# Optimization experiments

Hardware: AMD Instinct MI355X
Metric: run time of the kernel (lower is better)

The kernel has to match this reference:

```python
import jax, jax.numpy as jnp
import numpy as np

KS = (10, 25, 50, 100)  # numbers of highest-scored tiles to average (eval mode averages over all)
CLAMP = 1e4


def setup_inputs() -> dict:
    key = jax.random.key(0)
    k1, k2, k3, k4, k5, k6, k7 = jax.random.split(key, 7)
    B, C, N, H, O = 8, 2048, 8000, 256, 1000
    x = jax.random.normal(k1, (B, C, N), dtype=jnp.float32)
    # Conv1d(kernel=1) weights == [out, in] matrices
    W0 = jax.random.normal(k2, (H, C), dtype=jnp.float32) * (1.0 / np.sqrt(C))
    b0 = jax.random.normal(k3, (H,), dtype=jnp.float32) * 0.01
    W1 = jax.random.normal(k4, (H, H), dtype=jnp.float32) * (1.0 / np.sqrt(H))
    b1 = jax.random.normal(k5, (H,), dtype=jnp.float32) * 0.01
    W2 = jax.random.normal(k6, (O, H), dtype=jnp.float32) * (1.0 / np.sqrt(H))
    b2 = jax.random.normal(k7, (O,), dtype=jnp.float32) * 0.01
    return {"x": x, "W0": W0, "b0": b0, "W1": W1, "b1": b1, "W2": W2, "b2": b2}


def reference(x, W0, b0, W1, b1, W2, b2):
    # x: [B, C, N] tile features. Eval-mode dropout is identity.
    # mask: tile is 'real' if its max feature > 0 (padding tiles are all-zero)
    mask = (jnp.max(x, axis=1, keepdims=True) > 0).astype(x.dtype)  # [B,1,N]
    # 1x1 conv stack (Conv1d kernel=1 == per-tile matmul)
    h = jnp.einsum('hc,bcn->bhn', W0, x) + b0[None, :, None]
    h = jnp.clip(jax.nn.relu(h), -CLAMP, CLAMP)
    h = jnp.einsum('hg,bgn->bhn', W1, h) + b1[None, :, None]
    h = jnp.clip(jax.nn.relu(h), -CLAMP, CLAMP)
    y = jnp.einsum('oh,bhn->bon', W2, h) + b2[None, :, None]  # [B,O,N]
    y = y * mask
    # top-kmax once (sorted descending); top-k for smaller k is a prefix slice
    kmax = max(KS)
    t, _ = jax.lax.top_k(y, kmax)  # [B,O,kmax]
    pred = jnp.zeros(y.shape[:2], dtype=y.dtype)  # [B,O]
    inv = 1.0 / len(KS)
    for k in KS:
        num = jnp.sum(t[:, :, :k] * mask[:, :, :k], axis=2)  # [B,O]
        den = jnp.sum(mask[:, :, :k], axis=2)                 # [B,1]
        pred = pred + (num / den) * inv
    return pred
```

## Files before the change

kernel.cpp:

```cpp
#include <hip/hip_runtime.h>
#include <hip/hip_bf16.h>
#include <stdint.h>

typedef __bf16 bf16;
typedef __bf16 bf16x8 __attribute__((ext_vector_type(8)));
typedef __bf16 bf16x4 __attribute__((ext_vector_type(4)));
typedef float  floatx4 __attribute__((ext_vector_type(4)));
typedef unsigned int uint32;

#define B_  8
#define C_  2048
#define N_  8000
#define H_  256
#define O_  1000
#define OP_ 1024

__device__ __forceinline__ void gll16(const void* g, void* l) {
  __builtin_amdgcn_global_load_lds((const __attribute__((address_space(1))) void*)g,
                                   (__attribute__((address_space(3))) void*)l, 16, 0, 0);
}

__global__ __launch_bounds__(256) void castw(const float* __restrict__ W0,
                                             const float* __restrict__ W1,
                                             const float* __restrict__ W2,
                                             bf16* __restrict__ W0b,
                                             bf16* __restrict__ W1b,
                                             bf16* __restrict__ W2b) {
  int idx = blockIdx.x * 256 + threadIdx.x;
  if (idx < 524288) {
    W0b[idx] = (bf16)W0[idx];
  } else if (idx < 524288 + 65536) {
    int i = idx - 524288;
    W1b[i] = (bf16)W1[i];
  } else {
    int i = idx - (524288 + 65536);
    int o = i >> 8, k = i & 255;
    W2b[i] = (o < O_) ? (bf16)W2[o * 256 + k] : (bf16)0.0f;
  }
}

__global__ __launch_bounds__(256) void gemm1(const float* __restrict__ x,
                                             const bf16* __restrict__ W0b,
                                             const float* __restrict__ bias0,
                                             bf16* __restrict__ h1T,
                                             float* __restrict__ maskb) {
  __shared__ union {
    struct { bf16 A[H_ * 32]; bf16 Bt[64 * 40]; } st;
    bf16 HT[64 * 264];
  } sm;
  __shared__ float sbias[256];
  __shared__ uint32 nflag[64];

  const int tid  = threadIdx.x;
  const int wave = tid >> 6, lane = tid & 63;
  const int l16  = lane & 15, l4 = lane >> 4;
  const int n0   = blockIdx.x * 64;
  const int b    = blockIdx.y;

  sbias[tid] = bias0[tid];
  if (tid < 64) nflag[tid] = 0;

  const int kp = tid >> 4;
  const int n4 = (tid & 15) * 4;
  const float* xbase = x + (size_t)b * C_ * N_ + n0 + n4;

  floatx4 acc[4][4];
  #pragma unroll
  for (int i = 0; i < 4; ++i)
    #pragma unroll
    for (int j = 0; j < 4; ++j)
      acc[i][j] = floatx4{0.f, 0.f, 0.f, 0.f};

  uint32 fl = 0;

  for (int k0 = 0; k0 < C_; k0 += 32) {
    #pragma unroll
    for (int i = 0; i < 4; ++i) {
      int c = i * 256 + tid;
      gll16(W0b + (size_t)(c >> 2) * C_ + k0 + (c & 3) * 8, &sm.st.A[c * 8]);
    }
    const float* xr = xbase + (size_t)(k0 + 2 * kp) * N_;
    float4 q0 = *(const float4*)xr;
    float4 q1 = *(const float4*)(xr + N_);
    float a0[4] = {q0.x, q0.y, q0.z, q0.w};
    float a1[4] = {q1.x, q1.y, q1.z, q1.w};
    uint32* bw = (uint32*)sm.st.Bt;
    #pragma unroll
    for (int i = 0; i < 4; ++i) {
      if (a0[i] > 0.f || a1[i] > 0.f) fl |= (1u << i);
      union { bf16 h[2]; uint32 u; } p;
      p.h[0] = (bf16)a0[i];
      p.h[1] = (bf16)a1[i];
      bw[(n4 + i) * 20 + kp] = p.u;
    }
    __syncthreads();

    bf16x8 af[4], bfr[4];
    #pragma unroll
    for (int mt = 0; mt < 4; ++mt)
      af[mt] = *(const bf16x8*)&sm.st.A[(wave * 64 + mt * 16 + l16) * 32 + l4 * 8];
    #pragma unroll
    for (int nt = 0; nt < 4; ++nt)
      bfr[nt] = *(const bf16x8*)&sm.st.Bt[(nt * 16 + l16) * 40 + l4 * 8];
    #pragma unroll
    for (int mt = 0; mt < 4; ++mt)
      #pragma unroll
      for (int nt = 0; nt < 4; ++nt)
        acc[mt][nt] = __builtin_amdgcn_mfma_f32_16x16x32_bf16(af[mt], bfr[nt], acc[mt][nt], 0, 0, 0);
    __syncthreads();
  }

  #pragma unroll
  for (int i = 0; i < 4; ++i)
    if (fl & (1u << i)) atomicOr(&nflag[n4 + i], 1u);
  __syncthreads();
  if (tid < 64) maskb[(size_t)b * N_ + n0 + tid] = nflag[tid] ? 1.f : 0.f;

  #pragma unroll
  for (int mt = 0; mt < 4; ++mt) {
    int m0 = wave * 64 + mt * 16 + l4 * 4;
    #pragma unroll
    for (int nt = 0; nt < 4; ++nt) {
      int n = nt * 16 + l16;
      bf16x4 hv;
      #pragma unroll
      for (int r = 0; r < 4; ++r) {
        float v = acc[mt][nt][r] + sbias[m0 + r];
        v = fminf(fmaxf(v, 0.f), 1.0e4f);
        hv[r] = (bf16)v;
      }
      *(bf16x4*)&sm.HT[n * 264 + m0] = hv;
    }
  }
  __syncthreads();
  {
    int n = tid >> 2, q = tid & 3;
    const char* src = (const char*)&sm.HT[n * 264 + q * 64];
    bf16* dst = h1T + ((size_t)b * N_ + n0 + n) * H_ + q * 64;
    #pragma unroll
    for (int j = 0; j < 8; ++j)
      *(uint4*)((char*)dst + j * 16) = *(const uint4*)(src + j * 16);
  }
}

template <int OUTL>
__global__ __launch_bounds__(256) void gemmA(const bf16* __restrict__ A,
                                             const float* __restrict__ bias, int biasLim,
                                             const bf16* __restrict__ Bt,
                                             const float* __restrict__ mk,
                                             bf16* __restrict__ outp) {
  __shared__ union {
    struct { bf16 A[256 * 32]; bf16 Bs[64 * 32]; } st;
    bf16 HT[64 * 264];
    bf16 YT[256 * 72];
  } sm;
  __shared__ float sbias[256];
  __shared__ float smk[64];

  const int tid  = threadIdx.x;
  const int wave = tid >> 6, lane = tid & 63;
  const int l16  = lane & 15, l4 = lane >> 4;
  const int n0   = blockIdx.x * 64;
  const int mb   = blockIdx.y;
  const int b    = blockIdx.z;
  const int m0g  = mb * 256;

  { int og = m0g + tid; sbias[tid] = (og < biasLim) ? bias[og] : 0.f; }
  if (OUTL && tid < 64) smk[tid] = mk[(size_t)b * N_ + n0 + tid];

  floatx4 acc[4][4];
  #pragma unroll
  for (int i = 0; i < 4; ++i)
    #pragma unroll
    for (int j = 0; j < 4; ++j)
      acc[i][j] = floatx4{0.f, 0.f, 0.f, 0.f};

  const bf16* Bbase = Bt + ((size_t)b * N_ + n0) * 256;

  for (int k0 = 0; k0 < 256; k0 += 32) {
    #pragma unroll
    for (int i = 0; i < 4; ++i) {
      int c = i * 256 + tid;
      gll16(A + (size_t)(m0g + (c >> 2)) * 256 + k0 + (c & 3) * 8, &sm.st.A[c * 8]);
    }
    gll16(Bbase + (size_t)(tid >> 2) * 256 + k0 + (tid & 3) * 8, &sm.st.Bs[tid * 8]);
    __syncthreads();

    bf16x8 af[4], bfr[4];
    #pragma unroll
    for (int mt = 0; mt < 4; ++mt)
      af[mt] = *(const bf16x8*)&sm.st.A[(wave * 64 + mt * 16 + l16) * 32 + l4 * 8];
    #pragma unroll
    for (int nt = 0; nt < 4; ++nt)
      bfr[nt] = *(const bf16x8*)&sm.st.Bs[(nt * 16 + l16) * 32 + l4 * 8];
    #pragma unroll
    for (int mt = 0; mt < 4; ++mt)
      #pragma unroll
      for (int nt = 0; nt < 4; ++nt)
        acc[mt][nt] = __builtin_amdgcn_mfma_f32_16x16x32_bf16(af[mt], bfr[nt], acc[mt][nt], 0, 0, 0);
    __syncthreads();
  }

  if constexpr (!OUTL) {
    #pragma unroll
    for (int mt = 0; mt < 4; ++mt) {
      int m0 = wave * 64 + mt * 16 + l4 * 4;
      #pragma unroll
      for (int nt = 0; nt < 4; ++nt) {
        int n = nt * 16 + l16;
        bf16x4 hv;
        #pragma unroll
        for (int r = 0; r < 4; ++r) {
          float v = acc[mt][nt][r] + sbias[m0 + r];
          v = fminf(fmaxf(v, 0.f), 1.0e4f);
          hv[r] = (bf16)v;
        }
        *(bf16x4*)&sm.HT[n * 264 + m0] = hv;
      }
    }
    __syncthreads();
    int n = tid >> 2, q = tid & 3;
    const char* src = (const char*)&sm.HT[n * 264 + q * 64];
    bf16* dst = outp + ((size_t)b * N_ + n0 + n) * H_ + q * 64;
    #pragma unroll
    for (int j = 0; j < 8; ++j)
      *(uint4*)((char*)dst + j * 16) = *(const uint4*)(src + j * 16);
  } else {
    #pragma unroll
    for (int mt = 0; mt < 4; ++mt) {
      int m0 = wave * 64 + mt * 16 + l4 * 4;
      #pragma unroll
      for (int nt = 0; nt < 4; ++nt) {
        int n = nt * 16 + l16;
        float m = smk[n];
        #pragma unroll
        for (int r = 0; r < 4; ++r) {
          float v = (acc[mt][nt][r] + sbias[m0 + r]) * m;
          sm.YT[(m0 + r) * 72 + n] = (bf16)v;
        }
      }
    }
    __syncthreads();
    bf16* dst = outp + ((size_t)b * OP_ + m0g + tid) * N_ + n0;
    const char* src = (const char*)&sm.YT[tid * 72];
    #pragma unroll
    for (int j = 0; j < 8; ++j)
      *(uint4*)((char*)dst + j * 16) = *(const uint4*)(src + j * 16);
  }
}

__global__ __launch_bounds__(64) void topk(const bf16* __restrict__ y,
                                           const float* __restrict__ maskb,
                                           float* __restrict__ out) {
  __shared__ uint32 cand[128];
  __shared__ float  sval[128];
  __shared__ float  m100[100];
  __shared__ int    gcnt;

  const int lane = threadIdx.x;
  const int o = blockIdx.x, b = blockIdx.y;

  const uint32* yw = (const uint32*)(y + ((size_t)b * OP_ + o) * N_);
  const float*  mr = maskb + (size_t)b * N_;

  if (lane == 0) gcnt = 0;
  m100[lane] = mr[lane];
  if (lane < 36) m100[64 + lane] = mr[64 + lane];

  uint32 khi[64], klo[64];
  #pragma unroll
  for (int i = 0; i < 16; ++i) {
    int base = i * 256 + lane * 4;
    bool real = (base < 4000);
    uint4 v = make_uint4(0u, 0u, 0u, 0u);
    if (real) v = *(const uint4*)(yw + base);
    uint32 ww[4] = {v.x, v.y, v.z, v.w};
    #pragma unroll
    for (int j = 0; j < 4; ++j) {
      uint32 w = ww[j];
      uint32 sgn = w & 0x80008000u;
      uint32 mskk = 0x80008000u | (sgn - (sgn >> 15));
      uint32 k = w ^ mskk;
      if (!real) k = 0u;
      khi[i * 4 + j] = k;
      klo[i * 4 + j] = k << 16;
    }
  }

  uint32 prefix = 0;
  #pragma unroll 1
  for (int bit = 15; bit >= 0; --bit) {
    uint32 T16 = (prefix | (1u << bit)) << 16;
    int c = 0, d = 0;
    #pragma unroll
    for (int r = 0; r < 64; ++r) {
      c += (khi[r] >= T16);
      d += (klo[r] >= T16);
    }
    c += d;
    #pragma unroll
    for (int m = 1; m < 64; m <<= 1) c += __shfl_xor(c, m, 64);
    if (c >= 100) prefix |= (1u << bit);
  }

  #pragma unroll
  for (int r = 0; r < 64; ++r) {
    uint32 h = khi[r] >> 16;
    uint32 l = khi[r] & 0xffffu;
    if (h > prefix) { int p = atomicAdd(&gcnt, 1); cand[p] = h; }
    if (l > prefix) { int p = atomicAdd(&gcnt, 1); cand[p] = l; }
  }
  __syncthreads();
  int cg = gcnt;
  for (int idx = lane; idx < 100; idx += 64)
    if (idx >= cg) cand[idx] = prefix;
  __syncthreads();

  for (int idx = lane; idx < 100; idx += 64) {
    uint32 ci = cand[idx];
    int rank = 0;
    for (int j = 0; j < 100; ++j) {
      uint32 cj = cand[j];
      rank += (cj > ci) || (cj == ci && j < idx);
    }
    uint32 bb = (ci & 0x8000u) ? (ci & 0x7fffu) : (~ci & 0xffffu);
    sval[rank] = __uint_as_float(bb << 16);
  }
  __syncthreads();

  if (lane == 0) {
    const int KSv[4] = {10, 25, 50, 100};
    float num = 0.f, den = 0.f, pred = 0.f;
    int ki = 0;
    for (int j = 0; j < 100; ++j) {
      num += sval[j] * m100[j];
      den += m100[j];
      if (j + 1 == KSv[ki]) { pred += 0.25f * num / den; ++ki; }
    }
    out[(size_t)b * O_ + o] = pred;
  }
}

extern "C" void kernel_launch(void* const* d_in, const int* in_sizes, int n_in,
                              void* d_out, int out_size, void* d_ws, size_t ws_size,
                              hipStream_t stream) {
  const float* x  = (const float*)d_in[0];
  const float* W0 = (const float*)d_in[1];
  const float* b0 = (const float*)d_in[2];
  const float* W1 = (const float*)d_in[3];
  const float* b1 = (const float*)d_in[4];
  const float* W2 = (const float*)d_in[5];
  const float* b2 = (const float*)d_in[6];
  float* out = (float*)d_out;

  char* ws = (char*)d_ws;
  bf16*  W0b  = (bf16*)(ws + 0);
  bf16*  W1b  = (bf16*)(ws + 1048576);
  bf16*  W2b  = (bf16*)(ws + 1179648);
  float* mk   = (float*)(ws + 1703936);
  bf16*  h1T  = (bf16*)(ws + 1959936);
  bf16*  h2T  = (bf16*)(ws + 34727936);
  bf16*  yb   = (bf16*)(ws + 67495936);

  castw<<<3328, 256, 0, stream>>>(W0, W1, W2, W0b, W1b, W2b);
  gemm1<<<dim3(125, 8), 256, 0, stream>>>(x, W0b, b0, h1T, mk);
  gemmA<0><<<dim3(125, 1, 8), 256, 0, stream>>>(W1b, b1, H_, h1T, nullptr, h2T);
  gemmA<1><<<dim3(125, 4, 8), 256, 0, stream>>>(W2b, b2, O_, h2T, mk, yb);
  topk<<<dim3(1000, 8), 64, 0, stream>>>(yb, mk, out);
}
```

Baseline: 986.6 us.

## Fuse second and third GEMMs keeping hidden activations in LDS

Merges the W1 and W2 GEMM kernels into one kernel. Each block computes its 64-tile slice of h2 into shared memory and then loops over the four output row blocks, so the bf16 h2 buffer is no longer written to and read back from global memory. The cost is fewer blocks for the W2 stage (1000 instead of 4000), with each block doing serial work and using more LDS, which may lower occupancy. The weight cast kernel is also vectorised to float4 loads, and topk drops its klo register array, recomputing the shifted key inside the counting loop.

Result: no change. 973.6 us (-1.3%).

```diff
diff --git a/kernel.cpp b/kernel.cpp
--- a/kernel.cpp
+++ b/kernel.cpp
@@ -26,17 +26,26 @@
                                              bf16* __restrict__ W0b,
                                              bf16* __restrict__ W1b,
                                              bf16* __restrict__ W2b) {
-  int idx = blockIdx.x * 256 + threadIdx.x;
-  if (idx < 524288) {
-    W0b[idx] = (bf16)W0[idx];
-  } else if (idx < 524288 + 65536) {
-    int i = idx - 524288;
-    W1b[i] = (bf16)W1[i];
+  int g = blockIdx.x * 256 + threadIdx.x;
+  float4 v;
+  bf16* dst;
+  if (g < 131072) {
+    v = ((const float4*)W0)[g];
+    dst = W0b + g * 4;
+  } else if (g < 147456) {
+    int i = g - 131072;
+    v = ((const float4*)W1)[i];
+    dst = W1b + i * 4;
   } else {
-    int i = idx - (524288 + 65536);
-    int o = i >> 8, k = i & 255;
-    W2b[i] = (o < O_) ? (bf16)W2[o * 256 + k] : (bf16)0.0f;
-  }
+    int i = g - 147456;
+    int o = i >> 6, k4 = i & 63;
+    if (o < O_) v = *(const float4*)(W2 + o * 256 + k4 * 4);
+    else        v = make_float4(0.f, 0.f, 0.f, 0.f);
+    dst = W2b + i * 4;
+  }
+  bf16x4 r;
+  r[0] = (bf16)v.x; r[1] = (bf16)v.y; r[2] = (bf16)v.z; r[3] = (bf16)v.w;
+  *(bf16x4*)dst = r;
 }
 
 __global__ __launch_bounds__(256) void gemm1(const float* __restrict__ x,
@@ -143,30 +152,30 @@
   }
 }
 
-template <int OUTL>
-__global__ __launch_bounds__(256) void gemmA(const bf16* __restrict__ A,
-                                             const float* __restrict__ bias, int biasLim,
-                                             const bf16* __restrict__ Bt,
-                                             const float* __restrict__ mk,
-                                             bf16* __restrict__ outp) {
+__global__ __launch_bounds__(256) void gemm23(const bf16* __restrict__ W1b,
+                                              const float* __restrict__ b1,
+                                              const bf16* __restrict__ W2b,
+                                              const float* __restrict__ b2,
+                                              const bf16* __restrict__ h1T,
+                                              const float* __restrict__ mk,
+                                              bf16* __restrict__ yb) {
   __shared__ union {
-    struct { bf16 A[256 * 32]; bf16 Bs[64 * 32]; } st;
-    bf16 HT[64 * 264];
-    bf16 YT[256 * 72];
-  } sm;
-  __shared__ float sbias[256];
+    struct { bf16 A[256 * 32]; bf16 Bs[64 * 32]; } p1;
+    bf16 A2[256 * 32];
+    bf16 YT[128 * 72];
+  } u;
+  __shared__ bf16 HT[64 * 264];
+  __shared__ float sb[256];
   __shared__ float smk[64];
 
   const int tid  = threadIdx.x;
   const int wave = tid >> 6, lane = tid & 63;
   const int l16  = lane & 15, l4 = lane >> 4;
   const int n0   = blockIdx.x * 64;
-  const int mb   = blockIdx.y;
-  const int b    = blockIdx.z;
-  const int m0g  = mb * 256;
-
-  { int og = m0g + tid; sbias[tid] = (og < biasLim) ? bias[og] : 0.f; }
-  if (OUTL && tid < 64) smk[tid] = mk[(size_t)b * N_ + n0 + tid];
+  const int b    = blockIdx.y;
+
+  sb[tid] = b1[tid];
+  if (tid < 64) smk[tid] = mk[(size_t)b * N_ + n0 + tid];
 
   floatx4 acc[4][4];
   #pragma unroll
@@ -175,24 +184,24 @@
     for (int j = 0; j < 4; ++j)
       acc[i][j] = floatx4{0.f, 0.f, 0.f, 0.f};
 
-  const bf16* Bbase = Bt + ((size_t)b * N_ + n0) * 256;
+  const bf16* Bbase = h1T + ((size_t)b * N_ + n0) * 256;
 
   for (int k0 = 0; k0 < 256; k0 += 32) {
     #pragma unroll
     for (int i = 0; i < 4; ++i) {
       int c = i * 256 + tid;
-      gll16(A + (size_t)(m0g + (c >> 2)) * 256 + k0 + (c & 3) * 8, &sm.st.A[c * 8]);
-    }
-    gll16(Bbase + (size_t)(tid >> 2) * 256 + k0 + (tid & 3) * 8, &sm.st.Bs[tid * 8]);
+      gll16(W1b + (size_t)(c >> 2) * 256 + k0 + (c & 3) * 8, &u.p1.A[c * 8]);
+    }
+    gll16(Bbase + (size_t)(tid >> 2) * 256 + k0 + (tid & 3) * 8, &u.p1.Bs[tid * 8]);
     __syncthreads();
 
     bf16x8 af[4], bfr[4];
     #pragma unroll
     for (int mt = 0; mt < 4; ++mt)
-      af[mt] = *(const bf16x8*)&sm.st.A[(wave * 64 + mt * 16 + l16) * 32 + l4 * 8];
+      af[mt] = *(const bf16x8*)&u.p1.A[(wave * 64 + mt * 16 + l16) * 32 + l4 * 8];
     #pragma unroll
     for (int nt = 0; nt < 4; ++nt)
-      bfr[nt] = *(const bf16x8*)&sm.st.Bs[(nt * 16 + l16) * 32 + l4 * 8];
+      bfr[nt] = *(const bf16x8*)&u.p1.Bs[(nt * 16 + l16) * 32 + l4 * 8];
     #pragma unroll
     for (int mt = 0; mt < 4; ++mt)
       #pragma unroll
@@ -201,51 +210,84 @@
     __syncthreads();
   }
 
-  if constexpr (!OUTL) {
-    #pragma unroll
-    for (int mt = 0; mt < 4; ++mt) {
-      int m0 = wave * 64 + mt * 16 + l4 * 4;
-      #pragma unroll
-      for (int nt = 0; nt < 4; ++nt) {
-        int n = nt * 16 + l16;
-        bf16x4 hv;
+  #pragma unroll
+  for (int mt = 0; mt < 4; ++mt) {
+    int m0 = wave * 64 + mt * 16 + l4 * 4;
+    #pragma unroll
+    for (int nt = 0; nt < 4; ++nt) {
+      int n = nt * 16 + l16;
+      bf16x4 hv;
+      #pragma unroll
+      for (int r = 0; r < 4; ++r) {
+        float v = acc[mt][nt][r] + sb[m0 + r];
+        v = fminf(fmaxf(v, 0.f), 1.0e4f);
+        hv[r] = (bf16)v;
+      }
+      *(bf16x4*)&HT[n * 264 + m0] = hv;
+    }
+  }
+  __syncthreads();
+
+  for (int mb = 0; mb < 4; ++mb) {
+    const int m0g = mb * 256;
+    { int og = m0g + tid; sb[tid] = (og < O_) ? b2[og] : 0.f; }
+
+    #pragma unroll
+    for (int i = 0; i < 4; ++i)
+      #pragma unroll
+      for (int j = 0; j < 4; ++j)
+        acc[i][j] = floatx4{0.f, 0.f, 0.f, 0.f};
+
+    for (int k0 = 0; k0 < 256; k0 += 32) {
+      #pragma unroll
+      for (int i = 0; i < 4; ++i) {
+        int c = i * 256 + tid;
+        gll16(W2b + (size_t)(m0g + (c >> 2)) * 256 + k0 + (c & 3) * 8, &u.A2[c * 8]);
+      }
+      __syncthreads();
+
+      bf16x8 af[4], bfr[4];
+      #pragma unroll
+      for (int mt = 0; mt < 4; ++mt)
+        af[mt] = *(const bf16x8*)&u.A2[(wave * 64 + mt * 16 + l16) * 32 + l4 * 8];
+      #pragma unroll
+      for (int nt = 0; nt < 4; ++nt)
+        bfr[nt] = *(const bf16x8*)&HT[(nt * 16 + l16) * 264 + k0 + l4 * 8];
+      #pragma unroll
+      for (int mt = 0; mt < 4; ++mt)
         #pragma unroll
-        for (int r = 0; r < 4; ++r) {
-          float v = acc[mt][nt][r] + sbias[m0 + r];
-          v = fminf(fmaxf(v, 0.f), 1.0e4f);
-          hv[r] = (bf16)v;
-        }
-        *(bf16x4*)&sm.HT[n * 264 + m0] = hv;
-      }
-    }
-    __syncthreads();
-    int n = tid >> 2, q = tid & 3;
-    const char* src = (const char*)&sm.HT[n * 264 + q * 64];
-    bf16* dst = outp + ((size_t)b * N_ + n0 + n) * H_ + q * 64;
-    #pragma unroll
-    for (int j = 0; j < 8; ++j)
-      *(uint4*)((char*)dst + j * 16) = *(const uint4*)(src + j * 16);
-  } else {
-    #pragma unroll
-    for (int mt = 0; mt < 4; ++mt) {
-      int m0 = wave * 64 + mt * 16 + l4 * 4;
-      #pragma unroll
-      for (int nt = 0; nt < 4; ++nt) {
-        int n = nt * 16 + l16;
-        float m = smk[n];
-        #pragma unroll
-        for (int r = 0; r < 4; ++r) {
-          float v = (acc[mt][nt][r] + sbias[m0 + r]) * m;
-          sm.YT[(m0 + r) * 72 + n] = (bf16)v;
+        for (int nt = 0; nt < 4; ++nt)
+          acc[mt][nt] = __builtin_amdgcn_mfma_f32_16x16x32_bf16(af[mt], bfr[nt], acc[mt][nt], 0, 0, 0);
+      __syncthreads();
+    }
+
+    #pragma unroll
+    for (int h = 0; h < 2; ++h) {
+      #pragma unroll
+      for (int mt = 0; mt < 4; ++mt) {
+        int m0 = wave * 64 + mt * 16 + l4 * 4;
+        if ((m0 >> 7) == h) {
+          #pragma unroll
+          for (int nt = 0; nt < 4; ++nt) {
+            int n = nt * 16 + l16;
+            float m = smk[n];
+            #pragma unroll
+            for (int r = 0; r < 4; ++r)
+              u.YT[(m0 - h * 128 + r) * 72 + n] = (bf16)((acc[mt][nt][r] + sb[m0 + r]) * m);
+          }
         }
       }
-    }
-    __syncthreads();
-    bf16* dst = outp + ((size_t)b * OP_ + m0g + tid) * N_ + n0;
-    const char* src = (const char*)&sm.YT[tid * 72];
-    #pragma unroll
-    for (int j = 0; j < 8; ++j)
-      *(uint4*)((char*)dst + j * 16) = *(const uint4*)(src + j * 16);
+      __syncthreads();
+      {
+        int row = tid >> 1, ch = tid & 1;
+        const char* src = (const char*)&u.YT[row * 72 + ch * 32];
+        bf16* dst = yb + ((size_t)b * OP_ + m0g + h * 128 + row) * N_ + n0 + ch * 32;
+        #pragma unroll
+        for (int j = 0; j < 4; ++j)
+          *(uint4*)((char*)dst + j * 16) = *(const uint4*)(src + j * 16);
+      }
+      __syncthreads();
+    }
   }
 }
 
@@ -267,7 +309,7 @@
   m100[lane] = mr[lane];
   if (lane < 36) m100[64 + lane] = mr[64 + lane];
 
-  uint32 khi[64], klo[64];
+  uint32 khi[64];
   #pragma unroll
   for (int i = 0; i < 16; ++i) {
     int base = i * 256 + lane * 4;
@@ -283,7 +325,6 @@
       uint32 k = w ^ mskk;
       if (!real) k = 0u;
       khi[i * 4 + j] = k;
-      klo[i * 4 + j] = k << 16;
     }
   }
 
@@ -291,13 +332,12 @@
   #pragma unroll 1
   for (int bit = 15; bit >= 0; --bit) {
     uint32 T16 = (prefix | (1u << bit)) << 16;
-    int c = 0, d = 0;
+    int c = 0;
     #pragma unroll
     for (int r = 0; r < 64; ++r) {
       c += (khi[r] >= T16);
-      d += (klo[r] >= T16);
-    }
-    c += d;
+      c += ((khi[r] << 16) >= T16);
+    }
     #pragma unroll
     for (int m = 1; m < 64; m <<= 1) c += __shfl_xor(c, m, 64);
     if (c >= 100) prefix |= (1u << bit);
@@ -359,12 +399,10 @@
   bf16*  W2b  = (bf16*)(ws + 1179648);
   float* mk   = (float*)(ws + 1703936);
   bf16*  h1T  = (bf16*)(ws + 1959936);
-  bf16*  h2T  = (bf16*)(ws + 34727936);
-  bf16*  yb   = (bf16*)(ws + 67495936);
-
-  castw<<<3328, 256, 0, stream>>>(W0, W1, W2, W0b, W1b, W2b);
+  bf16*  yb   = (bf16*)(ws + 34727936);
+
+  castw<<<832, 256, 0, stream>>>(W0, W1, W2, W0b, W1b, W2b);
   gemm1<<<dim3(125, 8), 256, 0, stream>>>(x, W0b, b0, h1T, mk);
-  gemmA<0><<<dim3(125, 1, 8), 256, 0, stream>>>(W1b, b1, H_, h1T, nullptr, h2T);
-  gemmA<1><<<dim3(125, 4, 8), 256, 0, stream>>>(W2b, b2, O_, h2T, mk, yb);
+  gemm23<<<dim3(125, 8), 256, 0, stream>>>(W1b, b1, W2b, b2, h1T, mk, yb);
   topk<<<dim3(1000, 8), 64, 0, stream>>>(yb, mk, out);
 }
```
